# Optimization experiments

Hardware: AMD Instinct MI355X
Metric: run time of the kernel (lower is better)

The kernel has to match this reference:

```python
import math
import jax, jax.numpy as jnp
import numpy as np

FACTOR = 1  # self.factor
B, L, H, E = 16, 2048, 8, 64


def setup_inputs() -> dict:
    key = jax.random.key(0)
    kq, kk, kv = jax.random.split(key, 3)
    queries = jax.random.normal(kq, (B, L, H, E), dtype=jnp.float32)
    keys = jax.random.normal(kk, (B, L, H, E), dtype=jnp.float32)
    values = jax.random.normal(kv, (B, L, H, E), dtype=jnp.float32)
    return {"queries": queries, "keys": keys, "values": values}


def reference(queries, keys, values):
    # AutoCorrelation forward, agg_mode='speed', inference path (train=False),
    # norm=False, Q == K == V lengths so the pad/truncate branch is a no-op.
    Bb, Ll, Hh, Ee = queries.shape
    # Permute to [B, H, E, L] as the torch code does before FFT / aggregation.
    qp = jnp.transpose(queries, (0, 2, 3, 1))
    kp = jnp.transpose(keys, (0, 2, 3, 1))
    vp = jnp.transpose(values, (0, 2, 3, 1))
    # (1) period-based dependency discovery: circular cross-correlation via FFT
    q_fft = jnp.fft.rfft(qp, axis=-1)
    k_fft = jnp.fft.rfft(kp, axis=-1)
    corr = jnp.fft.irfft(q_fft * jnp.conj(k_fft), n=Ll, axis=-1)  # [B,H,E,L]
    # (2) time delay aggregation (speed mode, inference):
    k = int(FACTOR * math.log(Ll))
    mean_r_qk = jnp.mean(corr, axis=(1, 2))  # mean over head then channel -> [B,L]
    r_qk_top, tao = jax.lax.top_k(mean_r_qk, k)  # [B,k]
    weights = jax.nn.softmax(r_qk_top, axis=-1)  # [B,k]
    # gather into values repeated twice along L  <=>  circular roll by tao
    idx = (jnp.arange(Ll)[None, None, :] + tao[:, :, None]) % Ll  # [B,k,L]
    # [B,1,H,E,L] gathered with [B,k,1,1,L] -> [B,k,H,E,L]
    gathered = jnp.take_along_axis(vp[:, None], idx[:, :, None, None, :], axis=-1)
    agg = jnp.einsum('bk,bkhel->bhel', weights, gathered)  # softmax-weighted sum
    # back to [B, L, H, E]
    return jnp.transpose(agg, (0, 3, 1, 2))
```

## Files before the change

kernel.cpp:

```cpp
#include <hip/hip_runtime.h>
#include <math.h>

#define LN      2048
#define LOG2L   11
#define BB      16
#define HE      512
#define KTOP    7
#define TWO_PI  6.283185307179586f
#define RC      0.70710678118654752f

#define SIG(e)  ((e) ^ (((e) >> 5) & 31))

struct c32 { float x, y; };
__device__ __forceinline__ c32 cmul(c32 a, c32 b) {
    return { a.x * b.x - a.y * b.y, a.x * b.y + a.y * b.x };
}
__device__ __forceinline__ c32 cadd(c32 a, c32 b) { return { a.x + b.x, a.y + b.y }; }
__device__ __forceinline__ c32 csub(c32 a, c32 b) { return { a.x - b.x, a.y - b.y }; }

__device__ __forceinline__ void dft4(c32 a, c32 b, c32 c, c32 d,
                                     c32& y0, c32& y1, c32& y2, c32& y3) {
    c32 t0 = cadd(a, c), t1 = csub(a, c);
    c32 t2 = cadd(b, d);
    c32 t3 = { b.y - d.y, d.x - b.x };
    y0 = cadd(t0, t2);
    y1 = cadd(t1, t3);
    y2 = csub(t0, t2);
    y3 = csub(t1, t3);
}

__device__ __forceinline__ void dft8(const c32* x, c32* y) {
    c32 e0, e1, e2, e3, o0, o1, o2, o3;
    dft4(x[0], x[2], x[4], x[6], e0, e1, e2, e3);
    dft4(x[1], x[3], x[5], x[7], o0, o1, o2, o3);
    c32 p1 = { RC * (o1.x + o1.y), RC * (o1.y - o1.x) };
    c32 p2 = { o2.y, -o2.x };
    c32 p3 = { RC * (o3.y - o3.x), -RC * (o3.x + o3.y) };
    y[0] = cadd(e0, o0); y[4] = csub(e0, o0);
    y[1] = cadd(e1, p1); y[5] = csub(e1, p1);
    y[2] = cadd(e2, p2); y[6] = csub(e2, p2);
    y[3] = cadd(e3, p3); y[7] = csub(e3, p3);
}

template<int LOG2M>
__device__ __forceinline__ void r8_stage_wg(float2* Z, int tid) {
    c32 v[8];
    const int j = tid;
    #pragma unroll
    for (int r = 0; r < 8; ++r) {
        float2 z = Z[SIG(j + (r << 8))];
        v[r] = { z.x, z.y };
    }
    c32 y[8];
    dft8(v, y);
    const int pm = j & ~((1 << LOG2M) - 1);
    float sn, cs;
    __sincosf(-(TWO_PI / (float)LN) * (float)pm, &sn, &cs);
    c32 base = { cs, sn };
    c32 t = base;
    #pragma unroll
    for (int kk = 1; kk < 8; ++kk) {
        y[kk] = cmul(y[kk], t);
        if (kk < 7) t = cmul(t, base);
    }
    __syncthreads();
    const int q_ = j & ((1 << LOG2M) - 1);
    const int ob = q_ + ((j - q_) << 3);
    #pragma unroll
    for (int kk = 0; kk < 8; ++kk) {
        Z[SIG(ob + (kk << LOG2M))] = make_float2(y[kk].x, y[kk].y);
    }
    __syncthreads();
}

__device__ __forceinline__ void r4_final_wg(float2* Z, int tid) {
    c32 v[2][4];
    #pragma unroll
    for (int u = 0; u < 2; ++u) {
        const int j = tid + (u << 8);
        #pragma unroll
        for (int r = 0; r < 4; ++r) {
            float2 z = Z[SIG(j + (r << 9))];
            v[u][r] = { z.x, z.y };
        }
    }
    __syncthreads();
    #pragma unroll
    for (int u = 0; u < 2; ++u) {
        const int j = tid + (u << 8);
        c32 y0, y1, y2, y3;
        dft4(v[u][0], v[u][1], v[u][2], v[u][3], y0, y1, y2, y3);
        Z[SIG(j)]        = make_float2(y0.x, y0.y);
        Z[SIG(j + 512)]  = make_float2(y1.x, y1.y);
        Z[SIG(j + 1024)] = make_float2(y2.x, y2.y);
        Z[SIG(j + 1536)] = make_float2(y3.x, y3.y);
    }
    __syncthreads();
}

__global__ __launch_bounds__(256) void transpose_pack_kernel(
    const float* __restrict__ q, const float* __restrict__ k,
    float* __restrict__ qT, float* __restrict__ kT) {
    __shared__ float2 tile[64][65];
    const int tid = threadIdx.x;
    const int bid = blockIdx.x;
    const int b  = bid >> 8;
    const int lt = (bid >> 3) & 31;
    const int ct = bid & 7;
    const int l0 = lt << 6, c0 = ct << 6;
    const int col = tid & 63, row = tid >> 6;
    #pragma unroll
    for (int rr = 0; rr < 16; ++rr) {
        const int r = (rr << 2) + row;
        const size_t src = ((size_t)(b * LN + l0 + r)) * HE + c0 + col;
        tile[r][col] = make_float2(q[src], k[src]);
    }
    __syncthreads();
    #pragma unroll
    for (int rr = 0; rr < 16; ++rr) {
        const int r = (rr << 2) + row;
        const float2 v = tile[col][r];
        const size_t dst = ((size_t)(b * HE + c0 + r)) * LN + l0 + col;
        qT[dst] = v.x;
        kT[dst] = v.y;
    }
}

__global__ __launch_bounds__(256) void fft_wg_kernel(
    const float* __restrict__ qT, const float* __restrict__ kT,
    float* __restrict__ spec ) {
    __shared__ float2 Z[LN];
    const int tid = threadIdx.x;
    const int wg  = blockIdx.x;
    const int b   = wg >> 7;
    const int c0  = (wg & 127) << 2;

    float accx[8], accy[8];
    #pragma unroll
    for (int i = 0; i < 8; ++i) { accx[i] = 0.f; accy[i] = 0.f; }

    #pragma unroll 1
    for (int ch = 0; ch < 4; ++ch) {
        const size_t base = ((size_t)(b * HE + c0 + ch)) << LOG2L;
        const float4* q4 = (const float4*)(qT + base);
        const float4* k4 = (const float4*)(kT + base);
        #pragma unroll
        for (int i = 0; i < 2; ++i) {
            const int i4 = tid + (i << 8);
            const float4 qv = q4[i4];
            const float4 kv = k4[i4];
            const int l = i4 << 2;
            Z[SIG(l)]     = make_float2(qv.x, kv.x);
            Z[SIG(l + 1)] = make_float2(qv.y, kv.y);
            Z[SIG(l + 2)] = make_float2(qv.z, kv.z);
            Z[SIG(l + 3)] = make_float2(qv.w, kv.w);
        }
        __syncthreads();

        r8_stage_wg<0>(Z, tid);
        r8_stage_wg<3>(Z, tid);
        r8_stage_wg<6>(Z, tid);
        r4_final_wg(Z, tid);

        #pragma unroll
        for (int i = 0; i < 8; ++i) {
            const int f = tid + (i << 8);
            const float2 zf = Z[SIG(f)];
            const float2 zm = Z[SIG((LN - f) & (LN - 1))];
            const float Qr = 0.5f * (zf.x + zm.x);
            const float Qi = 0.5f * (zf.y - zm.y);
            const float Kr = 0.5f * (zf.y + zm.y);
            const float Ki = -0.5f * (zf.x - zm.x);
            accx[i] += Qr * Kr + Qi * Ki;
            accy[i] += Qi * Kr - Qr * Ki;
        }
        __syncthreads();
    }
    #pragma unroll
    for (int i = 0; i < 8; ++i) {
        const int f = tid + (i << 8);
        atomicAdd(&spec[((size_t)b * LN + f) * 2 + 0], accx[i]);
        atomicAdd(&spec[((size_t)b * LN + f) * 2 + 1], accy[i]);
    }
}

template<int LOG2M>
__device__ __forceinline__ void r8_stage(float2* Z, int lane) {
    c32 v[32];
    #pragma unroll
    for (int u = 0; u < 4; ++u) {
        const int j = lane + (u << 6);
        #pragma unroll
        for (int r = 0; r < 8; ++r) {
            float2 z = Z[SIG(j + (r << 8))];
            v[(u << 3) + r] = { z.x, z.y };
        }
    }
    c32 y[32];
    #pragma unroll
    for (int u = 0; u < 4; ++u) {
        const int j  = lane + (u << 6);
        const int pm = j & ~((1 << LOG2M) - 1);
        dft8(&v[u << 3], &y[u << 3]);
        float sn, cs;
        __sincosf(-(TWO_PI / (float)LN) * (float)pm, &sn, &cs);
        c32 base = { cs, sn };
        c32 t = base;
        #pragma unroll
        for (int kk = 1; kk < 8; ++kk) {
            y[(u << 3) + kk] = cmul(y[(u << 3) + kk], t);
            if (kk < 7) t = cmul(t, base);
        }
    }
    __syncthreads();
    #pragma unroll
    for (int u = 0; u < 4; ++u) {
        const int j  = lane + (u << 6);
        const int q_ = j & ((1 << LOG2M) - 1);
        const int ob = q_ + ((j - q_) << 3);
        #pragma unroll
        for (int kk = 0; kk < 8; ++kk) {
            c32 yy = y[(u << 3) + kk];
            Z[SIG(ob + (kk << LOG2M))] = make_float2(yy.x, yy.y);
        }
    }
    __syncthreads();
}

__device__ __forceinline__ void r4_final(float2* Z, int lane) {
    c32 v[32];
    #pragma unroll
    for (int u = 0; u < 8; ++u) {
        const int j = lane + (u << 6);
        #pragma unroll
        for (int r = 0; r < 4; ++r) {
            float2 z = Z[SIG(j + (r << 9))];
            v[(u << 2) + r] = { z.x, z.y };
        }
    }
    __syncthreads();
    #pragma unroll
    for (int u = 0; u < 8; ++u) {
        const int j = lane + (u << 6);
        c32 y0, y1, y2, y3;
        dft4(v[u << 2], v[(u << 2) + 1], v[(u << 2) + 2], v[(u << 2) + 3],
             y0, y1, y2, y3);
        Z[SIG(j)]        = make_float2(y0.x, y0.y);
        Z[SIG(j + 512)]  = make_float2(y1.x, y1.y);
        Z[SIG(j + 1024)] = make_float2(y2.x, y2.y);
        Z[SIG(j + 1536)] = make_float2(y3.x, y3.y);
    }
    __syncthreads();
}

__global__ __launch_bounds__(256) void fft_fused_kernel(
    const float* __restrict__ qg, const float* __restrict__ kg,
    float* __restrict__ spec) {
    __shared__ float2 zb[4][LN];
    const int t    = threadIdx.x;
    const int bid  = blockIdx.x;
    const int wgid = ((bid & 7) << 8) | (bid >> 3);
    const int b    = wgid >> 7;
    const int c0   = (wgid & 127) << 2;
    #pragma unroll
    for (int i = 0; i < 8; ++i) {
        const int l = t + (i << 8);
        const size_t base = (size_t)(b * LN + l) * HE + c0;
        const float4 qv = *(const float4*)(qg + base);
        const float4 kv = *(const float4*)(kg + base);
        const int sl = SIG(l);
        zb[0][sl] = make_float2(qv.x, kv.x);
        zb[1][sl] = make_float2(qv.y, kv.y);
        zb[2][sl] = make_float2(qv.z, kv.z);
        zb[3][sl] = make_float2(qv.w, kv.w);
    }
    __syncthreads();
    const int w    = t >> 6;
    const int lane = t & 63;
    float2* Z = zb[w];
    r8_stage<0>(Z, lane);
    r8_stage<3>(Z, lane);
    r8_stage<6>(Z, lane);
    r4_final(Z, lane);
    float sx[32], sy[32];
    #pragma unroll
    for (int i = 0; i < 32; ++i) {
        const int f = lane + (i << 6);
        const float2 zf = Z[SIG(f)];
        const float2 zm = Z[SIG((LN - f) & (LN - 1))];
        const float Qr = 0.5f * (zf.x + zm.x);
        const float Qi = 0.5f * (zf.y - zm.y);
        const float Kr = 0.5f * (zf.y + zm.y);
        const float Ki = -0.5f * (zf.x - zm.x);
        sx[i] = Qr * Kr + Qi * Ki;
        sy[i] = Qi * Kr - Qr * Ki;
    }
    __syncthreads();
    #pragma unroll
    for (int i = 0; i < 32; ++i) {
        const int f = lane + (i << 6);
        Z[SIG(f)] = make_float2(sx[i], sy[i]);
    }
    __syncthreads();
    #pragma unroll
    for (int i = 0; i < 8; ++i) {
        const int f  = t + (i << 8);
        const int sf = SIG(f);
        const float rx = zb[0][sf].x + zb[1][sf].x + zb[2][sf].x + zb[3][sf].x;
        const float ry = zb[0][sf].y + zb[1][sf].y + zb[2][sf].y + zb[3][sf].y;
        atomicAdd(&spec[((size_t)b * LN + f) * 2 + 0], rx);
        atomicAdd(&spec[((size_t)b * LN + f) * 2 + 1], ry);
    }
}

__device__ __forceinline__ unsigned bitrev11(unsigned x) {
    return __brev(x) >> (32 - LOG2L);
}

__global__ __launch_bounds__(256) void icorr_topk_kernel(
    const float* __restrict__ spec, float* __restrict__ wts, int* __restrict__ tao) {
    __shared__ float2 zbuf[LN];
    __shared__ float2 tw[LN / 2];
    __shared__ float  cr[LN];
    __shared__ float  rv[256];
    __shared__ int    ri[256];
    __shared__ float  topv[KTOP];
    __shared__ int    topi[KTOP];
    const int tid = threadIdx.x;
    const int b   = blockIdx.x;
    for (int p = tid; p < LN / 2; p += 256) {
        float s, c;
        sincosf(-TWO_PI * (float)p / (float)LN, &s, &c);
        tw[p] = make_float2(c, s);
    }
    for (int f = tid; f < LN; f += 256) {
        float sr = spec[((size_t)b * LN + f) * 2 + 0];
        float si = spec[((size_t)b * LN + f) * 2 + 1];
        zbuf[bitrev11((unsigned)f)] = make_float2(sr, -si);
    }
    __syncthreads();
    for (int s = 0; s < LOG2L; ++s) {
        const int half = 1 << s;
        for (int j = tid; j < LN / 2; j += 256) {
            const int grp = j >> s;
            const int pos = j & (half - 1);
            const int i0  = (grp << (s + 1)) + pos;
            const int i1  = i0 + half;
            const float2 w = tw[pos << (LOG2L - 1 - s)];
            float2 a  = zbuf[i0];
            float2 bv = zbuf[i1];
            float tr = w.x * bv.x - w.y * bv.y;
            float ti = w.x * bv.y + w.y * bv.x;
            zbuf[i0] = make_float2(a.x + tr, a.y + ti);
            zbuf[i1] = make_float2(a.x - tr, a.y - ti);
        }
        __syncthreads();
    }
    const float scale = 1.0f / ((float)LN * (float)HE);
    for (int t = tid; t < LN; t += 256) cr[t] = zbuf[t].x * scale;
    __syncthreads();
    for (int it = 0; it < KTOP; ++it) {
        float mv = -INFINITY;
        int   mi = 0;
        for (int t = tid; t < LN; t += 256) {
            float v = cr[t];
            if (v > mv) { mv = v; mi = t; }
        }
        rv[tid] = mv; ri[tid] = mi;
        __syncthreads();
        for (int off = 128; off > 0; off >>= 1) {
            if (tid < off) {
                float ov = rv[tid + off]; int oi = ri[tid + off];
                if (ov > rv[tid] || (ov == rv[tid] && oi < ri[tid])) {
                    rv[tid] = ov; ri[tid] = oi;
                }
            }
            __syncthreads();
        }
        if (tid == 0) {
            topv[it] = rv[0];
            topi[it] = ri[0];
            cr[ri[0]] = -INFINITY;
        }
        __syncthreads();
    }
    if (tid == 0) {
        float m = topv[0];
        float s = 0.f;
        float ex[KTOP];
        for (int j = 0; j < KTOP; ++j) { ex[j] = __expf(topv[j] - m); s += ex[j]; }
        float inv = 1.0f / s;
        for (int j = 0; j < KTOP; ++j) {
            wts[b * 8 + j] = ex[j] * inv;
            tao[b * 8 + j] = topi[j];
        }
    }
}

__global__ __launch_bounds__(256) void gather_kernel(
    const float* __restrict__ v, const float* __restrict__ wts,
    const int* __restrict__ tao, float* __restrict__ out) {
    __shared__ float lw[KTOP];
    __shared__ int   lt[KTOP];
    const int tid = threadIdx.x;
    const int bid = blockIdx.x;
    const int wg  = ((bid & 7) << 11) | (bid >> 3);
    const long long idx = (long long)wg * 256 + tid;
    const int c4 = (int)(idx & 127);
    const int l  = (int)((idx >> 7) & (LN - 1));
    const int b  = (int)(idx >> 18);
    if (tid < KTOP) {
        lw[tid] = wts[b * 8 + tid];
        lt[tid] = tao[b * 8 + tid];
    }
    __syncthreads();
    const float4* v4 = (const float4*)v;
    float4 a = make_float4(0.f, 0.f, 0.f, 0.f);
    #pragma unroll
    for (int j = 0; j < KTOP; ++j) {
        int ls = (l + lt[j]) & (LN - 1);
        float4 x = v4[((size_t)b * LN + ls) * 128 + c4];
        float w = lw[j];
        a.x += w * x.x; a.y += w * x.y; a.z += w * x.z; a.w += w * x.w;
    }
    ((float4*)out)[idx] = a;
}

extern "C" void kernel_launch(void* const* d_in, const int* in_sizes, int n_in,
                              void* d_out, int out_size, void* d_ws, size_t ws_size,
                              hipStream_t stream) {
    const float* q = (const float*)d_in[0];
    const float* k = (const float*)d_in[1];
    const float* v = (const float*)d_in[2];
    float* out = (float*)d_out;

    const size_t nT   = (size_t)BB * HE * LN;
    const size_t need = nT * 4 + (size_t)BB * LN * 2 * 4 + (size_t)BB * 8 * 8;

    if (ws_size >= need) {
        float* kT   = (float*)d_ws;
        float* spec = kT + nT;
        float* wts  = spec + (size_t)BB * LN * 2;
        int*   tao  = (int*)(wts + BB * 8);
        float* qT   = out;

        hipMemsetAsync(spec, 0, (size_t)BB * LN * 2 * sizeof(float), stream);
        transpose_pack_kernel<<<BB * 32 * 8, 256, 0, stream>>>(q, k, qT, kT);
        fft_wg_kernel<<<BB * (HE / 4), 256, 0, stream>>>(qT, kT, spec);
        icorr_topk_kernel<<<BB, 256, 0, stream>>>(spec, wts, tao);
        const int n4 = BB * LN * HE / 4;
        gather_kernel<<<n4 / 256, 256, 0, stream>>>(v, wts, tao, out);
    } else {
        float* spec = (float*)d_ws;
        float* wts  = spec + (size_t)BB * LN * 2;
        int*   tao  = (int*)(wts + BB * 8);
        hipMemsetAsync(spec, 0, (size_t)BB * LN * 2 * sizeof(float), stream);
        fft_fused_kernel<<<BB * (HE / 4), 256, 0, stream>>>(q, k, spec);
        icorr_topk_kernel<<<BB, 256, 0, stream>>>(spec, wts, tao);
        const int n4 = BB * LN * HE / 4;
        gather_kernel<<<n4 / 256, 256, 0, stream>>>(v, wts, tao, out);
    }
}
```

Measured before the change: 175.2 us.

## Load first FFT stage from registers, precompute twiddles, exploit Hermitian symmetry

The first radix-8 stage now reads directly from global memory into registers, skipping one shared-memory round trip and its barriers. Per-stage twiddles are computed once per thread before the channel loop instead of on every stage call. Only the non-negative half spectrum (f <= 1024) is accumulated and atomically added. The inverse kernel rebuilds the negative frequencies by conjugate symmetry. This halves the cross-spectrum atomics and accumulation work, at the cost of more live registers for the twiddle tables.

```diff
diff --git a/kernel.cpp b/kernel.cpp
--- a/kernel.cpp
+++ b/kernel.cpp
@@ -42,34 +42,35 @@
     y[3] = cadd(e3, p3); y[7] = csub(e3, p3);
 }
 
+__device__ __forceinline__ void mk_tw(int pm, c32* W) {
+    float sn, cs;
+    __sincosf(-(TWO_PI / (float)LN) * (float)pm, &sn, &cs);
+    const c32 w1 = { cs, sn };
+    const c32 w2 = cmul(w1, w1);
+    const c32 w3 = cmul(w1, w2);
+    const c32 w4 = cmul(w2, w2);
+    W[0] = w1; W[1] = w2; W[2] = w3; W[3] = w4;
+    W[4] = cmul(w1, w4); W[5] = cmul(w2, w4); W[6] = cmul(w3, w4);
+}
+
 template<int LOG2M>
-__device__ __forceinline__ void r8_stage_wg(float2* Z, int tid) {
+__device__ __forceinline__ void r8_ld(float2* Z, int tid, const c32* TW) {
     c32 v[8];
-    const int j = tid;
     #pragma unroll
     for (int r = 0; r < 8; ++r) {
-        float2 z = Z[SIG(j + (r << 8))];
+        float2 z = Z[SIG(tid + (r << 8))];
         v[r] = { z.x, z.y };
     }
     c32 y[8];
     dft8(v, y);
-    const int pm = j & ~((1 << LOG2M) - 1);
-    float sn, cs;
-    __sincosf(-(TWO_PI / (float)LN) * (float)pm, &sn, &cs);
-    c32 base = { cs, sn };
-    c32 t = base;
-    #pragma unroll
-    for (int kk = 1; kk < 8; ++kk) {
-        y[kk] = cmul(y[kk], t);
-        if (kk < 7) t = cmul(t, base);
-    }
-    __syncthreads();
-    const int q_ = j & ((1 << LOG2M) - 1);
-    const int ob = q_ + ((j - q_) << 3);
-    #pragma unroll
-    for (int kk = 0; kk < 8; ++kk) {
+    #pragma unroll
+    for (int kk = 1; kk < 8; ++kk) y[kk] = cmul(y[kk], TW[kk - 1]);
+    __syncthreads();
+    const int q_ = tid & ((1 << LOG2M) - 1);
+    const int ob = q_ + ((tid - q_) << 3);
+    #pragma unroll
+    for (int kk = 0; kk < 8; ++kk)
         Z[SIG(ob + (kk << LOG2M))] = make_float2(y[kk].x, y[kk].y);
-    }
     __syncthreads();
 }
 
@@ -126,7 +127,7 @@
     }
 }
 
-__global__ __launch_bounds__(256) void fft_wg_kernel(
+__global__ __launch_bounds__(256) void fft_reg0_kernel(
     const float* __restrict__ qT, const float* __restrict__ kT,
     float* __restrict__ spec ) {
     __shared__ float2 Z[LN];
@@ -135,38 +136,45 @@
     const int b   = wg >> 7;
     const int c0  = (wg & 127) << 2;
 
-    float accx[8], accy[8];
-    #pragma unroll
-    for (int i = 0; i < 8; ++i) { accx[i] = 0.f; accy[i] = 0.f; }
+    c32 TW0[7], TW1[7], TW2[7];
+    mk_tw(tid, TW0);
+    mk_tw(tid & ~7, TW1);
+    mk_tw(tid & ~63, TW2);
+
+    float accx[4], accy[4];
+    #pragma unroll
+    for (int i = 0; i < 4; ++i) { accx[i] = 0.f; accy[i] = 0.f; }
+    float a1024 = 0.f;
 
     #pragma unroll 1
     for (int ch = 0; ch < 4; ++ch) {
         const size_t base = ((size_t)(b * HE + c0 + ch)) << LOG2L;
-        const float4* q4 = (const float4*)(qT + base);
-        const float4* k4 = (const float4*)(kT + base);
-        #pragma unroll
-        for (int i = 0; i < 2; ++i) {
-            const int i4 = tid + (i << 8);
-            const float4 qv = q4[i4];
-            const float4 kv = k4[i4];
-            const int l = i4 << 2;
-            Z[SIG(l)]     = make_float2(qv.x, kv.x);
-            Z[SIG(l + 1)] = make_float2(qv.y, kv.y);
-            Z[SIG(l + 2)] = make_float2(qv.z, kv.z);
-            Z[SIG(l + 3)] = make_float2(qv.w, kv.w);
-        }
+        c32 v[8];
+        #pragma unroll
+        for (int r = 0; r < 8; ++r) {
+            v[r].x = qT[base + tid + (r << 8)];
+            v[r].y = kT[base + tid + (r << 8)];
+        }
+        c32 y[8];
+        dft8(v, y);
+        #pragma unroll
+        for (int kk = 1; kk < 8; ++kk) y[kk] = cmul(y[kk], TW0[kk - 1]);
         __syncthreads();
-
-        r8_stage_wg<0>(Z, tid);
-        r8_stage_wg<3>(Z, tid);
-        r8_stage_wg<6>(Z, tid);
+        #pragma unroll
+        for (int kk = 0; kk < 8; ++kk)
+            Z[SIG((tid << 3) + kk)] = make_float2(y[kk].x, y[kk].y);
+        __syncthreads();
+
+        r8_ld<3>(Z, tid, TW1);
+        r8_ld<6>(Z, tid, TW2);
         r4_final_wg(Z, tid);
 
         #pragma unroll
-        for (int i = 0; i < 8; ++i) {
+        for (int i = 0; i < 4; ++i) {
             const int f = tid + (i << 8);
+            const int g = (LN - f) & (LN - 1);
             const float2 zf = Z[SIG(f)];
-            const float2 zm = Z[SIG((LN - f) & (LN - 1))];
+            const float2 zm = Z[SIG(g)];
             const float Qr = 0.5f * (zf.x + zm.x);
             const float Qi = 0.5f * (zf.y - zm.y);
             const float Kr = 0.5f * (zf.y + zm.y);
@@ -174,14 +182,19 @@
             accx[i] += Qr * Kr + Qi * Ki;
             accy[i] += Qi * Kr - Qr * Ki;
         }
-        __syncthreads();
-    }
-    #pragma unroll
-    for (int i = 0; i < 8; ++i) {
+        if (tid == 0) {
+            const float2 zf = Z[SIG(1024)];
+            a1024 += zf.x * zf.y;
+        }
+    }
+    #pragma unroll
+    for (int i = 0; i < 4; ++i) {
         const int f = tid + (i << 8);
         atomicAdd(&spec[((size_t)b * LN + f) * 2 + 0], accx[i]);
         atomicAdd(&spec[((size_t)b * LN + f) * 2 + 1], accy[i]);
     }
+    if (tid == 0)
+        atomicAdd(&spec[((size_t)b * LN + 1024) * 2 + 0], a1024);
 }
 
 template<int LOG2M>
@@ -305,11 +318,13 @@
     #pragma unroll
     for (int i = 0; i < 8; ++i) {
         const int f  = t + (i << 8);
-        const int sf = SIG(f);
-        const float rx = zb[0][sf].x + zb[1][sf].x + zb[2][sf].x + zb[3][sf].x;
-        const float ry = zb[0][sf].y + zb[1][sf].y + zb[2][sf].y + zb[3][sf].y;
-        atomicAdd(&spec[((size_t)b * LN + f) * 2 + 0], rx);
-        atomicAdd(&spec[((size_t)b * LN + f) * 2 + 1], ry);
+        if (f <= 1024) {
+            const int sf = SIG(f);
+            const float rx = zb[0][sf].x + zb[1][sf].x + zb[2][sf].x + zb[3][sf].x;
+            const float ry = zb[0][sf].y + zb[1][sf].y + zb[2][sf].y + zb[3][sf].y;
+            atomicAdd(&spec[((size_t)b * LN + f) * 2 + 0], rx);
+            atomicAdd(&spec[((size_t)b * LN + f) * 2 + 1], ry);
+        }
     }
 }
 
@@ -334,9 +349,11 @@
         tw[p] = make_float2(c, s);
     }
     for (int f = tid; f < LN; f += 256) {
-        float sr = spec[((size_t)b * LN + f) * 2 + 0];
-        float si = spec[((size_t)b * LN + f) * 2 + 1];
-        zbuf[bitrev11((unsigned)f)] = make_float2(sr, -si);
+        const int  fs  = (f <= 1024) ? f : (LN - f);
+        const float sg = (f <= 1024) ? -1.f : 1.f;
+        float sr = spec[((size_t)b * LN + fs) * 2 + 0];
+        float si = spec[((size_t)b * LN + fs) * 2 + 1];
+        zbuf[bitrev11((unsigned)f)] = make_float2(sr, sg * si);
     }
     __syncthreads();
     for (int s = 0; s < LOG2L; ++s) {
@@ -446,7 +463,7 @@
 
         hipMemsetAsync(spec, 0, (size_t)BB * LN * 2 * sizeof(float), stream);
         transpose_pack_kernel<<<BB * 32 * 8, 256, 0, stream>>>(q, k, qT, kT);
-        fft_wg_kernel<<<BB * (HE / 4), 256, 0, stream>>>(qT, kT, spec);
+        fft_reg0_kernel<<<BB * (HE / 4), 256, 0, stream>>>(qT, kT, spec);
         icorr_topk_kernel<<<BB, 256, 0, stream>>>(spec, wts, tao);
         const int n4 = BB * LN * HE / 4;
         gather_kernel<<<n4 / 256, 256, 0, stream>>>(v, wts, tao, out);
```

Measured after the change: 172.5 us. About the same (-1.5%).
